# Performance work log

Measured on AMD Instinct MI355X. Metric: run time of the kernel, lower is better.

The kernel has to match this reference:

```python
import jax, jax.numpy as jnp
import numpy as np

B, T, D, H = 256, 256, 512, 8
HD = D // H  # 64


def _rope_tables(t, hd):
    pos = jnp.arange(t, dtype=jnp.float32)
    inv_freq = 1.0 / (10000.0 ** (jnp.arange(0, hd, 2, dtype=jnp.float32) / hd))
    ang = pos[:, None] * inv_freq[None, :]            # (T, hd/2)
    cos = jnp.repeat(jnp.cos(ang), 2, axis=-1)        # (T, hd) interleaved pairs
    sin = jnp.repeat(jnp.sin(ang), 2, axis=-1)
    return cos, sin


def setup_inputs() -> dict:
    key = jax.random.key(0)
    k1, k2, k3 = jax.random.split(key, 3)
    x = jax.random.normal(k1, (B, T, D), dtype=jnp.float32)
    cos, sin = _rope_tables(T, HD)
    Wqkv = jax.random.normal(k2, (3 * D, D), dtype=jnp.float32) * 0.02
    Wout = jax.random.normal(k3, (D, D), dtype=jnp.float32) * 0.02
    return {"x": x, "cos": cos, "sin": sin, "Wqkv": Wqkv, "Wout": Wout}


def _apply_rope(x, cos, sin):
    # x: (B, T, H, hd); cos/sin: (T, hd)
    x1 = x[..., 0::2]
    x2 = x[..., 1::2]
    rot = jnp.stack((-x2, x1), axis=-1).reshape(x.shape)  # interleaved rotate
    return x * cos[None, :, None, :] + rot * sin[None, :, None, :]


def reference(x, cos, sin, Wqkv, Wout):
    b, t, d = x.shape
    qkv = (x @ Wqkv.T).reshape(b, t, 3, H, HD)
    q, k, v = qkv[:, :, 0], qkv[:, :, 1], qkv[:, :, 2]   # (B, T, H, hd)
    q = _apply_rope(q, cos[:t], sin[:t])
    k = _apply_rope(k, cos[:t], sin[:t])
    q = q.transpose(0, 2, 1, 3)  # (B, H, T, hd)
    k = k.transpose(0, 2, 1, 3)
    v = v.transpose(0, 2, 1, 3)
    scale = 1.0 / jnp.sqrt(jnp.float32(HD))
    scores = jnp.einsum('bhqd,bhkd->bhqk', q, k) * scale
    causal = jnp.arange(t)[:, None] >= jnp.arange(t)[None, :]  # (T, T)
    scores = jnp.where(causal[None, None], scores, jnp.finfo(scores.dtype).min)
    att = jax.nn.softmax(scores, axis=-1)
    out = jnp.einsum('bhqk,bhkd->bhqd', att, v)          # (B, H, T, hd)
    out = out.transpose(0, 2, 1, 3).reshape(b, t, d)
    return out @ Wout.T
```

## Files before the change

### kernel.cpp

```cpp
#include <hip/hip_runtime.h>

typedef float floatx4 __attribute__((ext_vector_type(4)));
typedef short short8 __attribute__((ext_vector_type(8)));
typedef unsigned short ushort_t;

#define AS1 __attribute__((address_space(1)))
#define AS3 __attribute__((address_space(3)))

__device__ __forceinline__ void gload_lds16(const ushort_t* g, ushort_t* l) {
    __builtin_amdgcn_global_load_lds((const AS1 unsigned int*)g, (AS3 unsigned int*)l, 16, 0, 0);
}

__device__ __forceinline__ ushort_t f2bf(float f) {
    union { float f; unsigned u; } v; v.f = f;
    unsigned r = v.u + 0x7FFFu + ((v.u >> 16) & 1u);
    return (ushort_t)(r >> 16);
}

#define KDIM 512
#define LOG2E 1.44269504f

#define XB_OFF   0ull
#define ATT_OFF  0ull
#define WQKV_OFF 33554432ull
#define WOUT_OFF 34340864ull
#define QB_OFF   34603008ull
#define KB_OFF   68157440ull
#define VB_OFF   101711872ull

__global__ __launch_bounds__(256) void convert_k(
    const float* __restrict__ x, const float* __restrict__ wqkv,
    const float* __restrict__ wout, ushort_t* __restrict__ dst)
{
    size_t i = (size_t)blockIdx.x * 256 + threadIdx.x;
    size_t e = i * 4;
    const float* s; size_t o;
    if (e < 33554432ull)      { s = x;    o = e; }
    else if (e < 34340864ull) { s = wqkv; o = e - 33554432ull; }
    else                      { s = wout; o = e - 34340864ull; }
    float4 v = *(const float4*)(s + o);
    ushort4 r;
    r.x = f2bf(v.x); r.y = f2bf(v.y); r.z = f2bf(v.z); r.w = f2bf(v.w);
    *(ushort4*)(dst + e) = r;
}


__device__ __forceinline__ void stage_tile(const ushort_t* __restrict__ Ag,
    const ushort_t* __restrict__ Bg, ushort_t* As, ushort_t* Bs,
    const int k0, const int tid)
{
#pragma unroll
    for (int rnd = 0; rnd < 2; rnd++) {
        const int e = rnd * 512 + tid;
        const int row = e >> 2, c8 = (e & 3) << 3;
        gload_lds16(Ag + (size_t)row * KDIM + k0 + c8, As + e * 8);
        gload_lds16(Bg + (size_t)row * KDIM + k0 + c8, Bs + e * 8);
    }
}

__device__ __forceinline__ void compute_tile(const ushort_t* Ab, const ushort_t* Bb,
    floatx4 (&acc)[8][4], const int wm, const int wn, const int l16, const int quad)
{
    short8 af[8], bfr[4];
#pragma unroll
    for (int mi = 0; mi < 8; mi++)
        af[mi] = *(const short8*)&Ab[(wm * 128 + mi * 16 + l16) * 32 + quad * 8];
#pragma unroll
    for (int ni = 0; ni < 4; ni++)
        bfr[ni] = *(const short8*)&Bb[(wn * 64 + ni * 16 + l16) * 32 + quad * 8];
    __builtin_amdgcn_s_setprio(1);
#pragma unroll
    for (int mi = 0; mi < 8; mi++)
#pragma unroll
        for (int ni = 0; ni < 4; ni++)
            acc[mi][ni] = __builtin_amdgcn_mfma_f32_16x16x32_bf16(
                af[mi], bfr[ni], acc[mi][ni], 0, 0, 0);
    __builtin_amdgcn_s_setprio(0);
}

#define PHASE_END(VMSTR)                               \
    asm volatile("s_waitcnt " VMSTR ::: "memory");     \
    __builtin_amdgcn_s_barrier();                      \
    __builtin_amdgcn_sched_barrier(0);

template <int EPI>
__global__ __launch_bounds__(512, 2) void gemm_bt(
    const ushort_t* __restrict__ A, const ushort_t* __restrict__ Bw,
    float* __restrict__ Cf,
    ushort_t* __restrict__ qout, ushort_t* __restrict__ kout, ushort_t* __restrict__ vout,
    const float* __restrict__ cosT, const float* __restrict__ sinT)
{
    __shared__ __align__(16) ushort_t As[4 * 8192];
    __shared__ __align__(16) ushort_t Bs[4 * 8192];
    const int bn = blockIdx.x, bm = blockIdx.y;
    const int tid = threadIdx.x;
    const int lane = tid & 63, wave = tid >> 6;
    const int wm = wave >> 2, wn = wave & 3;
    const int quad = lane >> 4, l16 = lane & 15;

    const ushort_t* Ag = A + (size_t)bm * 256 * KDIM;
    const ushort_t* Bg = Bw + (size_t)bn * 256 * KDIM;

    floatx4 acc[8][4] = {};

    stage_tile(Ag, Bg, As, Bs, 0, tid);
    stage_tile(Ag, Bg, As + 8192, Bs + 8192, 32, tid);
    stage_tile(Ag, Bg, As + 16384, Bs + 16384, 64, tid);
    PHASE_END("vmcnt(8)")

#pragma unroll 1
    for (int t = 0; t < 13; t++) {
        const int pb = (t + 3) & 3;
        stage_tile(Ag, Bg, As + pb * 8192, Bs + pb * 8192, (t + 3) * 32, tid);
        compute_tile(As + (t & 3) * 8192, Bs + (t & 3) * 8192, acc, wm, wn, l16, quad);
        PHASE_END("vmcnt(8)")
    }
    compute_tile(As + 1 * 8192, Bs + 1 * 8192, acc, wm, wn, l16, quad);
    PHASE_END("vmcnt(4)")
    compute_tile(As + 2 * 8192, Bs + 2 * 8192, acc, wm, wn, l16, quad);
    PHASE_END("vmcnt(0)")
    compute_tile(As + 3 * 8192, Bs + 3 * 8192, acc, wm, wn, l16, quad);

    if constexpr (EPI == 1) {
        const int n_base = bn * 256 + wn * 64;
        const int qkv = n_base >> 9;
        ushort_t* dst = (qkv == 0) ? qout : (qkv == 1 ? kout : vout);
#pragma unroll
        for (int mi = 0; mi < 8; mi++) {
            const int m = bm * 256 + wm * 128 + mi * 16 + quad * 4;
#pragma unroll
            for (int ni = 0; ni < 4; ni++) {
                const int n = n_base + ni * 16 + l16;
                const int nw = n & 511, hd = n & 63;
#pragma unroll
                for (int r = 0; r < 4; r++) {
                    const int mm = m + r, tt = mm & 255;
                    const size_t dsti = (size_t)mm * 512 + nw;
                    float val = acc[mi][ni][r];
                    if (qkv == 2) {
                        dst[dsti] = f2bf(val);
                    } else {
                        float partner = __shfl_xor(val, 1);
                        float c = cosT[tt * 64 + hd], s = sinT[tt * 64 + hd];
                        float o = val * c + ((hd & 1) ? partner : -partner) * s;
                        dst[dsti] = (qkv == 0) ? f2bf(o * 0.125f) : f2bf(o);
                    }
                }
            }
        }
    } else {
#pragma unroll
        for (int mi = 0; mi < 8; mi++) {
            const int m = bm * 256 + wm * 128 + mi * 16 + quad * 4;
#pragma unroll
            for (int ni = 0; ni < 4; ni++) {
                const int n = bn * 256 + wn * 64 + ni * 16 + l16;
#pragma unroll
                for (int r = 0; r < 4; r++)
                    Cf[(size_t)(m + r) * 512 + n] = acc[mi][ni][r];
            }
        }
    }
}

__global__ __launch_bounds__(256) void attn_k(
    const ushort_t* __restrict__ qb, const ushort_t* __restrict__ kb,
    const ushort_t* __restrict__ vb, ushort_t* __restrict__ attb)
{
    __shared__ __align__(16) ushort_t Ks[256 * 72];
    __shared__ __align__(16) ushort_t Vt[64 * 264];
    __shared__ __align__(16) ushort_t Ps[4 * 32 * 40];

    const int blk = blockIdx.x;
    const int qt = blk & 1, bh = blk >> 1;
    const int b = bh >> 3, h = bh & 7;
    const int tid = threadIdx.x, lane = tid & 63, w = tid >> 6;
    const int quad = lane >> 4, l16 = lane & 15;
    const int q0 = qt * 128;
    const int kend = q0 + 128;

    const ushort_t* Kg = kb + ((size_t)b * 256) * 512 + h * 64;
    const ushort_t* Vg = vb + ((size_t)b * 256) * 512 + h * 64;
    const ushort_t* Qg = qb + ((size_t)b * 256) * 512 + h * 64;

    for (int e8 = tid; e8 < kend * 8; e8 += 256) {
        int t = e8 >> 3, c = (e8 & 7) << 3;
        *(short8*)&Ks[t * 72 + c] = *(const short8*)&Kg[t * 512 + c];
        short8 vv = *(const short8*)&Vg[t * 512 + c];
#pragma unroll
        for (int j = 0; j < 8; j++) Vt[(c + j) * 264 + t] = ((const ushort_t*)&vv)[j];
    }
    __syncthreads();

    short8 qf[2][2];
#pragma unroll
    for (int mi = 0; mi < 2; mi++)
#pragma unroll
        for (int kk = 0; kk < 2; kk++)
            qf[mi][kk] = *(const short8*)&Qg[(size_t)(q0 + w * 32 + mi * 16 + l16) * 512 + kk * 32 + quad * 8];

    float lsum[2][4] = {};
    floatx4 o_[2][4] = {};

    ushort_t* Pw = &Ps[w * 32 * 40];
    const int ktdiag = qt * 4 + w;

    for (int kt = 0; kt <= ktdiag; kt++) {
        const bool diag = (kt == ktdiag);
        floatx4 s_[2][2] = {};
#pragma unroll
        for (int kk = 0; kk < 2; kk++) {
            short8 kf0 = *(const short8*)&Ks[(kt * 32 + l16) * 72 + kk * 32 + quad * 8];
            short8 kf1 = *(const short8*)&Ks[(kt * 32 + 16 + l16) * 72 + kk * 32 + quad * 8];
#pragma unroll
            for (int mi = 0; mi < 2; mi++) {
                s_[mi][0] = __builtin_amdgcn_mfma_f32_16x16x32_bf16(qf[mi][kk], kf0, s_[mi][0], 0, 0, 0);
                s_[mi][1] = __builtin_amdgcn_mfma_f32_16x16x32_bf16(qf[mi][kk], kf1, s_[mi][1], 0, 0, 0);
            }
        }
#pragma unroll
        for (int mi = 0; mi < 2; mi++) {
#pragma unroll
            for (int r = 0; r < 4; r++) {
                float p0 = exp2f(s_[mi][0][r] * LOG2E);
                float p1 = exp2f(s_[mi][1][r] * LOG2E);
                if (diag) {
                    const int rl = mi * 16 + quad * 4 + r;
                    if (l16 > rl)      p0 = 0.f;
                    if (l16 + 16 > rl) p1 = 0.f;
                }
                lsum[mi][r] += p0 + p1;
                const int rowL = mi * 16 + quad * 4 + r;
                Pw[rowL * 40 + l16] = f2bf(p0);
                Pw[rowL * 40 + 16 + l16] = f2bf(p1);
            }
        }
        __asm__ volatile("s_waitcnt lgkmcnt(0)" ::: "memory");
        short8 pf[2];
#pragma unroll
        for (int mi = 0; mi < 2; mi++)
            pf[mi] = *(const short8*)&Pw[(mi * 16 + l16) * 40 + quad * 8];
#pragma unroll
        for (int vni = 0; vni < 4; vni++) {
            short8 vf = *(const short8*)&Vt[(vni * 16 + l16) * 264 + kt * 32 + quad * 8];
#pragma unroll
            for (int mi = 0; mi < 2; mi++)
                o_[mi][vni] = __builtin_amdgcn_mfma_f32_16x16x32_bf16(pf[mi], vf, o_[mi][vni], 0, 0, 0);
        }
    }

#pragma unroll
    for (int mi = 0; mi < 2; mi++) {
#pragma unroll
        for (int r = 0; r < 4; r++) {
            float rs = lsum[mi][r];
            rs += __shfl_xor(rs, 1);
            rs += __shfl_xor(rs, 2);
            rs += __shfl_xor(rs, 4);
            rs += __shfl_xor(rs, 8);
            const float inv = 1.f / rs;
            const int t = q0 + w * 32 + mi * 16 + quad * 4 + r;
            const size_t base = ((size_t)(b * 256 + t)) * 512 + h * 64;
#pragma unroll
            for (int vni = 0; vni < 4; vni++)
                attb[base + vni * 16 + l16] = f2bf(o_[mi][vni][r] * inv);
        }
    }
}

extern "C" void kernel_launch(void* const* d_in, const int* in_sizes, int n_in,
                              void* d_out, int out_size, void* d_ws, size_t ws_size,
                              hipStream_t stream) {
    const float* x    = (const float*)d_in[0];
    const float* cosT = (const float*)d_in[1];
    const float* sinT = (const float*)d_in[2];
    const float* wqkv = (const float*)d_in[3];
    const float* wout = (const float*)d_in[4];
    float* out = (float*)d_out;
    ushort_t* ws = (ushort_t*)d_ws;

    ushort_t* xb    = ws + XB_OFF;
    ushort_t* wqkvb = ws + WQKV_OFF;
    ushort_t* woutb = ws + WOUT_OFF;
    ushort_t* qbp   = ws + QB_OFF;
    ushort_t* kbp   = ws + KB_OFF;
    ushort_t* vbp   = ws + VB_OFF;
    ushort_t* attb  = ws + ATT_OFF;

    convert_k<<<33792, 256, 0, stream>>>(x, wqkv, wout, ws);
    gemm_bt<1><<<dim3(6, 256), 512, 0, stream>>>(xb, wqkvb, nullptr, qbp, kbp, vbp, cosT, sinT);
    attn_k<<<4096, 256, 0, stream>>>(qbp, kbp, vbp, attb);
    gemm_bt<0><<<dim3(2, 256), 512, 0, stream>>>(attb, woutb, out, nullptr, nullptr, nullptr, nullptr, nullptr);
}
```

Baseline: 662.4 us.

## Restructure GEMM main loop into 64-wide k-tiles with interleaved half-stage loads

New measurement: 641.9 us. 1.03x faster.

```diff
diff --git a/kernel.cpp b/kernel.cpp
--- a/kernel.cpp
+++ b/kernel.cpp
@@ -19,6 +19,7 @@
 
 #define KDIM 512
 #define LOG2E 1.44269504f
+#define LGKM0 do { asm volatile("s_waitcnt lgkmcnt(0)" ::: "memory"); __builtin_amdgcn_sched_barrier(0); } while (0)
 
 #define XB_OFF   0ull
 #define ATT_OFF  0ull
@@ -45,43 +46,17 @@
 }
 
 
-__device__ __forceinline__ void stage_tile(const ushort_t* __restrict__ Ag,
-    const ushort_t* __restrict__ Bg, ushort_t* As, ushort_t* Bs,
-    const int k0, const int tid)
+__device__ __forceinline__ void stage_half(const ushort_t* __restrict__ G,
+    ushort_t* L, int u, int kh, int tid)
 {
+    const int c0 = u * 64 + kh * 32;
 #pragma unroll
     for (int rnd = 0; rnd < 2; rnd++) {
         const int e = rnd * 512 + tid;
         const int row = e >> 2, c8 = (e & 3) << 3;
-        gload_lds16(Ag + (size_t)row * KDIM + k0 + c8, As + e * 8);
-        gload_lds16(Bg + (size_t)row * KDIM + k0 + c8, Bs + e * 8);
-    }
-}
-
-__device__ __forceinline__ void compute_tile(const ushort_t* Ab, const ushort_t* Bb,
-    floatx4 (&acc)[8][4], const int wm, const int wn, const int l16, const int quad)
-{
-    short8 af[8], bfr[4];
-#pragma unroll
-    for (int mi = 0; mi < 8; mi++)
-        af[mi] = *(const short8*)&Ab[(wm * 128 + mi * 16 + l16) * 32 + quad * 8];
-#pragma unroll
-    for (int ni = 0; ni < 4; ni++)
-        bfr[ni] = *(const short8*)&Bb[(wn * 64 + ni * 16 + l16) * 32 + quad * 8];
-    __builtin_amdgcn_s_setprio(1);
-#pragma unroll
-    for (int mi = 0; mi < 8; mi++)
-#pragma unroll
-        for (int ni = 0; ni < 4; ni++)
-            acc[mi][ni] = __builtin_amdgcn_mfma_f32_16x16x32_bf16(
-                af[mi], bfr[ni], acc[mi][ni], 0, 0, 0);
-    __builtin_amdgcn_s_setprio(0);
-}
-
-#define PHASE_END(VMSTR)                               \
-    asm volatile("s_waitcnt " VMSTR ::: "memory");     \
-    __builtin_amdgcn_s_barrier();                      \
-    __builtin_amdgcn_sched_barrier(0);
+        gload_lds16(G + (size_t)row * KDIM + c0 + c8, L + e * 8);
+    }
+}
 
 template <int EPI>
 __global__ __launch_bounds__(512, 2) void gemm_bt(
@@ -90,8 +65,8 @@
     ushort_t* __restrict__ qout, ushort_t* __restrict__ kout, ushort_t* __restrict__ vout,
     const float* __restrict__ cosT, const float* __restrict__ sinT)
 {
-    __shared__ __align__(16) ushort_t As[4 * 8192];
-    __shared__ __align__(16) ushort_t Bs[4 * 8192];
+    __shared__ __align__(16) ushort_t As[2 * 2 * 8192];
+    __shared__ __align__(16) ushort_t Bs[2 * 2 * 8192];
     const int bn = blockIdx.x, bm = blockIdx.y;
     const int tid = threadIdx.x;
     const int lane = tid & 63, wave = tid >> 6;
@@ -103,50 +78,139 @@
 
     floatx4 acc[8][4] = {};
 
-    stage_tile(Ag, Bg, As, Bs, 0, tid);
-    stage_tile(Ag, Bg, As + 8192, Bs + 8192, 32, tid);
-    stage_tile(Ag, Bg, As + 16384, Bs + 16384, 64, tid);
-    PHASE_END("vmcnt(8)")
+    stage_half(Bg, Bs + 0,     0, 0, tid);
+    stage_half(Ag, As + 0,     0, 0, tid);
+    stage_half(Bg, Bs + 8192,  0, 1, tid);
+    stage_half(Ag, As + 8192,  0, 1, tid);
+    asm volatile("s_waitcnt vmcnt(4)" ::: "memory");
+    stage_half(Bg, Bs + 16384,        1, 0, tid);
+    stage_half(Ag, As + 16384,        1, 0, tid);
+    stage_half(Bg, Bs + 16384 + 8192, 1, 1, tid);
+    asm volatile("s_waitcnt vmcnt(6)" ::: "memory");
+    __builtin_amdgcn_s_barrier();
+
+    auto ktile_body = [&](int u, int mode) {
+        const int db = u & 1;
+        const ushort_t* A0 = As + db * 16384;
+        const ushort_t* A1 = A0 + 8192;
+        const ushort_t* B0 = Bs + db * 16384;
+        const ushort_t* B1 = B0 + 8192;
+        short8 af[4], bfr[4];
+
+#pragma unroll
+        for (int i = 0; i < 4; i++)
+            af[i] = *(const short8*)&A0[(wm * 128 + i * 16 + l16) * 32 + quad * 8];
+#pragma unroll
+        for (int j = 0; j < 4; j++)
+            bfr[j] = *(const short8*)&B0[(wn * 64 + j * 16 + l16) * 32 + quad * 8];
+        if (mode < 2) stage_half(Ag, As + ((u + 1) & 1) * 16384 + 8192, u + 1, 1, tid);
+        __builtin_amdgcn_s_barrier();
+        LGKM0;
+        __builtin_amdgcn_s_setprio(1);
+#pragma unroll
+        for (int i = 0; i < 4; i++)
+#pragma unroll
+            for (int j = 0; j < 4; j++)
+                acc[i][j] = __builtin_amdgcn_mfma_f32_16x16x32_bf16(af[i], bfr[j], acc[i][j], 0, 0, 0);
+        __builtin_amdgcn_s_setprio(0);
+        __builtin_amdgcn_s_barrier();
+
+#pragma unroll
+        for (int i = 0; i < 4; i++)
+            af[i] = *(const short8*)&A0[(wm * 128 + (4 + i) * 16 + l16) * 32 + quad * 8];
+        if (mode == 0) stage_half(Bg, Bs + db * 16384, u + 2, 0, tid);
+        __builtin_amdgcn_s_barrier();
+        LGKM0;
+        __builtin_amdgcn_s_setprio(1);
+#pragma unroll
+        for (int i = 0; i < 4; i++)
+#pragma unroll
+            for (int j = 0; j < 4; j++)
+                acc[4 + i][j] = __builtin_amdgcn_mfma_f32_16x16x32_bf16(af[i], bfr[j], acc[4 + i][j], 0, 0, 0);
+        __builtin_amdgcn_s_setprio(0);
+        __builtin_amdgcn_s_barrier();
+
+#pragma unroll
+        for (int i = 0; i < 4; i++)
+            af[i] = *(const short8*)&A1[(wm * 128 + i * 16 + l16) * 32 + quad * 8];
+#pragma unroll
+        for (int j = 0; j < 4; j++)
+            bfr[j] = *(const short8*)&B1[(wn * 64 + j * 16 + l16) * 32 + quad * 8];
+        if (mode == 0) stage_half(Ag, As + db * 16384, u + 2, 0, tid);
+        __builtin_amdgcn_s_barrier();
+        LGKM0;
+        __builtin_amdgcn_s_setprio(1);
+#pragma unroll
+        for (int i = 0; i < 4; i++)
+#pragma unroll
+            for (int j = 0; j < 4; j++)
+                acc[i][j] = __builtin_amdgcn_mfma_f32_16x16x32_bf16(af[i], bfr[j], acc[i][j], 0, 0, 0);
+        __builtin_amdgcn_s_setprio(0);
+        __builtin_amdgcn_s_barrier();
+
+#pragma unroll
+        for (int i = 0; i < 4; i++)
+            af[i] = *(const short8*)&A1[(wm * 128 + (4 + i) * 16 + l16) * 32 + quad * 8];
+        if (mode == 0) stage_half(Bg, Bs + db * 16384 + 8192, u + 2, 1, tid);
+        __builtin_amdgcn_s_barrier();
+        LGKM0;
+        __builtin_amdgcn_s_setprio(1);
+#pragma unroll
+        for (int i = 0; i < 4; i++)
+#pragma unroll
+            for (int j = 0; j < 4; j++)
+                acc[4 + i][j] = __builtin_amdgcn_mfma_f32_16x16x32_bf16(af[i], bfr[j], acc[4 + i][j], 0, 0, 0);
+        __builtin_amdgcn_s_setprio(0);
+        if (mode == 0)      { asm volatile("s_waitcnt vmcnt(6)" ::: "memory"); }
+        else if (mode == 1) { asm volatile("s_waitcnt vmcnt(0)" ::: "memory"); }
+        __builtin_amdgcn_s_barrier();
+    };
 
 #pragma unroll 1
-    for (int t = 0; t < 13; t++) {
-        const int pb = (t + 3) & 3;
-        stage_tile(Ag, Bg, As + pb * 8192, Bs + pb * 8192, (t + 3) * 32, tid);
-        compute_tile(As + (t & 3) * 8192, Bs + (t & 3) * 8192, acc, wm, wn, l16, quad);
-        PHASE_END("vmcnt(8)")
-    }
-    compute_tile(As + 1 * 8192, Bs + 1 * 8192, acc, wm, wn, l16, quad);
-    PHASE_END("vmcnt(4)")
-    compute_tile(As + 2 * 8192, Bs + 2 * 8192, acc, wm, wn, l16, quad);
-    PHASE_END("vmcnt(0)")
-    compute_tile(As + 3 * 8192, Bs + 3 * 8192, acc, wm, wn, l16, quad);
+    for (int u = 0; u < 6; u++) ktile_body(u, 0);
+    ktile_body(6, 1);
+    ktile_body(7, 2);
 
     if constexpr (EPI == 1) {
         const int n_base = bn * 256 + wn * 64;
         const int qkv = n_base >> 9;
         ushort_t* dst = (qkv == 0) ? qout : (qkv == 1 ? kout : vout);
+        ushort_t* Ep = (wave < 4) ? (As + wave * 8192) : (Bs + (wave - 4) * 8192);
 #pragma unroll
         for (int mi = 0; mi < 8; mi++) {
-            const int m = bm * 256 + wm * 128 + mi * 16 + quad * 4;
 #pragma unroll
             for (int ni = 0; ni < 4; ni++) {
-                const int n = n_base + ni * 16 + l16;
-                const int nw = n & 511, hd = n & 63;
 #pragma unroll
                 for (int r = 0; r < 4; r++) {
-                    const int mm = m + r, tt = mm & 255;
-                    const size_t dsti = (size_t)mm * 512 + nw;
+                    const int row = mi * 16 + quad * 4 + r;
+                    const int m = bm * 256 + wm * 128 + row;
+                    const int tt = m & 255;
+                    const int n = n_base + ni * 16 + l16;
+                    const int hd = n & 63;
                     float val = acc[mi][ni][r];
+                    float o;
                     if (qkv == 2) {
-                        dst[dsti] = f2bf(val);
+                        o = val;
                     } else {
                         float partner = __shfl_xor(val, 1);
                         float c = cosT[tt * 64 + hd], s = sinT[tt * 64 + hd];
-                        float o = val * c + ((hd & 1) ? partner : -partner) * s;
-                        dst[dsti] = (qkv == 0) ? f2bf(o * 0.125f) : f2bf(o);
+                        o = val * c + ((hd & 1) ? partner : -partner) * s;
+                        if (qkv == 0) o *= 0.125f;
                     }
+                    const int colp = (ni * 16 + l16) ^ (((row >> 2) & 3) << 4);
+                    Ep[row * 64 + colp] = f2bf(o);
                 }
             }
+        }
+        LGKM0;
+#pragma unroll
+        for (int t = 0; t < 16; t++) {
+            const int row = t * 8 + (lane >> 3);
+            const int c0 = (lane & 7) * 8;
+            const int colp = c0 ^ (((row >> 2) & 3) << 4);
+            short8 v = *(const short8*)&Ep[row * 64 + colp];
+            const int m = bm * 256 + wm * 128 + row;
+            *(short8*)&dst[(size_t)m * 512 + (n_base & 511) + c0] = v;
         }
     } else {
 #pragma unroll
```
